# Performance work log

Measured on AMD Instinct MI355X. Metric: run time of the kernel, lower is better.

Reference implementation:

```python
import jax, jax.numpy as jnp
import numpy as np
import math

B, S, KV, D, H = 4, 512, 4096, 1024, 16
HD = D // H  # head_dim = 64


def setup_inputs() -> dict:
    key = jax.random.key(0)
    ks = jax.random.split(key, 12)
    scale = 0.02
    return {
        "x": jax.random.normal(ks[0], (B, S, D), dtype=jnp.float32),
        "xa": jax.random.normal(ks[1], (B, KV, D), dtype=jnp.float32),
        "Wq": jax.random.normal(ks[2], (D, D), dtype=jnp.float32) * scale,
        "bq": jax.random.normal(ks[3], (D,), dtype=jnp.float32) * scale,
        "Wk": jax.random.normal(ks[4], (D, D), dtype=jnp.float32) * scale,  # key has no bias
        "Wv": jax.random.normal(ks[5], (D, D), dtype=jnp.float32) * scale,
        "bv": jax.random.normal(ks[6], (D,), dtype=jnp.float32) * scale,
        "Wo": jax.random.normal(ks[7], (D, D), dtype=jnp.float32) * scale,
        "bo": jax.random.normal(ks[8], (D,), dtype=jnp.float32) * scale,
        "cache_k": jnp.zeros((B, H, KV, HD), dtype=jnp.float32),
        "cache_v": jnp.zeros((B, H, KV, HD), dtype=jnp.float32),
    }


def reference(x, xa, Wq, bq, Wk, Wv, bv, Wo, bo, cache_k, cache_v):
    bsz, seq_len, _ = x.shape
    kv_len = xa.shape[1]
    # projections (torch nn.Linear convention: y = x @ W^T + b)
    q = (x @ Wq.T + bq).reshape(bsz, seq_len, H, HD).transpose(0, 2, 1, 3)   # [B,H,S,HD]
    k = (xa @ Wk.T).reshape(bsz, kv_len, H, HD).transpose(0, 2, 1, 3)        # [B,H,KV,HD]
    v = (xa @ Wv.T + bv).reshape(bsz, kv_len, H, HD).transpose(0, 2, 1, 3)   # [B,H,KV,HD]
    # prefill path: scatter k/v into positions [0, kv_len) of the cache
    updated_k = cache_k.at[:, :, :kv_len, :].set(k)
    updated_v = cache_v.at[:, :, :kv_len, :].set(v)
    # attention over full cache, fp32 softmax as in the original
    scores = jnp.einsum('bhqd,bhkd->bhqk', q, updated_k) / math.sqrt(HD)
    probs = jax.nn.softmax(scores.astype(jnp.float32), axis=-1).astype(q.dtype)
    attn = jnp.einsum('bhqk,bhkd->bhqd', probs, updated_v)                   # [B,H,S,HD]
    attn = attn.transpose(0, 2, 1, 3).reshape(bsz, seq_len, H * HD)
    out = attn @ Wo.T + bo
    return out, updated_k, updated_v
```

## Files before the change

kernel.cpp:

```cpp
#include <hip/hip_runtime.h>
#include <hip/hip_bf16.h>

using u16 = unsigned short;
typedef __bf16 bf16x8 __attribute__((ext_vector_type(8)));
typedef float f32x4 __attribute__((ext_vector_type(4)));

#define SB 4
#define SS 512
#define SKV 4096
#define SD 1024
#define SH 16
#define SHD 64
#define NSPLIT 4
#define NROWS 32768

__device__ inline u16 f2bf(float f){
  __hip_bfloat16 h = __float2bfloat16(f);
  return __builtin_bit_cast(u16, h);
}

__device__ inline bf16x8 ld_frag_g(const u16* p){
  uint4 v = *reinterpret_cast<const uint4*>(p);
  return __builtin_bit_cast(bf16x8, v);
}

__device__ inline bf16x8 ld_frag_lds(const char* base, int ob){
  uint4 v = *reinterpret_cast<const uint4*>(base + ob);
  return __builtin_bit_cast(bf16x8, v);
}

__global__ __launch_bounds__(256) void cast_kernel(const float* __restrict__ src,
                                                   u16* __restrict__ dst, int n4){
  int i = blockIdx.x * 256 + threadIdx.x;
  if (i < n4){
    float4 f = reinterpret_cast<const float4*>(src)[i];
    ushort4 u;
    u.x = f2bf(f.x); u.y = f2bf(f.y); u.z = f2bf(f.z); u.w = f2bf(f.w);
    reinterpret_cast<ushort4*>(dst)[i] = u;
  }
}

enum { MODE_Q = 0, MODE_K = 1, MODE_V = 2, MODE_OUT = 3 };

template<int MODE>
__global__ __launch_bounds__(256) void gemm_bt(const u16* __restrict__ A,
                                               const u16* __restrict__ W,
                                               const float* __restrict__ bias,
                                               float* __restrict__ outF,
                                               u16* __restrict__ outB)
{
  __shared__ u16 As[128*64];
  __shared__ u16 Bs[128*64];
  const int tid  = threadIdx.x;
  const int lane = tid & 63;
  const int wm   = ((tid >> 6) >> 1) * 64;
  const int wn   = ((tid >> 6) & 1) * 64;
  const long rowBase = (long)blockIdx.x * 128;
  const long colBase = (long)blockIdx.y * 128;

  f32x4 acc[4][4];
#pragma unroll
  for (int i = 0; i < 4; i++)
#pragma unroll
    for (int j = 0; j < 4; j++)
      acc[i][j] = (f32x4){0.f, 0.f, 0.f, 0.f};

  for (int kt = 0; kt < 16; ++kt){
    __syncthreads();
#pragma unroll
    for (int i = 0; i < 4; i++){
      int u = tid + i * 256;
      int r = u >> 3, c = u & 7;
      uint4 va = *reinterpret_cast<const uint4*>(A + (rowBase + r) * 1024 + kt * 64 + c * 8);
      uint4 vw = *reinterpret_cast<const uint4*>(W + (colBase + r) * 1024 + kt * 64 + c * 8);
      int ob = (r * 128 + c * 16) ^ ((r & 7) << 4);
      *reinterpret_cast<uint4*>(reinterpret_cast<char*>(As) + ob) = va;
      *reinterpret_cast<uint4*>(reinterpret_cast<char*>(Bs) + ob) = vw;
    }
    __syncthreads();
#pragma unroll
    for (int kk = 0; kk < 2; kk++){
      bf16x8 af[4], bfr[4];
#pragma unroll
      for (int mi = 0; mi < 4; mi++){
        int row = wm + mi * 16 + (lane & 15);
        int ob = (row * 128 + kk * 64 + (lane >> 4) * 16) ^ ((row & 7) << 4);
        af[mi] = __builtin_bit_cast(bf16x8,
                 *reinterpret_cast<const uint4*>(reinterpret_cast<const char*>(As) + ob));
      }
#pragma unroll
      for (int ni = 0; ni < 4; ni++){
        int row = wn + ni * 16 + (lane & 15);
        int ob = (row * 128 + kk * 64 + (lane >> 4) * 16) ^ ((row & 7) << 4);
        bfr[ni] = __builtin_bit_cast(bf16x8,
                 *reinterpret_cast<const uint4*>(reinterpret_cast<const char*>(Bs) + ob));
      }
#pragma unroll
      for (int mi = 0; mi < 4; mi++)
#pragma unroll
        for (int ni = 0; ni < 4; ni++)
          acc[mi][ni] = __builtin_amdgcn_mfma_f32_16x16x32_bf16(af[mi], bfr[ni], acc[mi][ni], 0, 0, 0);
    }
  }

#pragma unroll
  for (int mi = 0; mi < 4; mi++){
#pragma unroll
    for (int ni = 0; ni < 4; ni++){
      long gn = colBase + wn + ni * 16 + (lane & 15);
      float bb = 0.f;
      if (MODE == MODE_Q || MODE == MODE_V || MODE == MODE_OUT) bb = bias[gn];
      if (MODE == MODE_V){
        long gmBase = rowBase + wm + mi * 16 + ((lane >> 4) << 2);
        long b = gmBase >> 12, kv = gmBase & 4095;
        long h = gn >> 6, hd = gn & 63;
        long fidx = ((b * SH + h) * SKV + kv) * SHD + hd;
        ushort4 pk;
        float v0 = acc[mi][ni][0] + bb; outF[fidx          ] = v0; pk.x = f2bf(v0);
        float v1 = acc[mi][ni][1] + bb; outF[fidx +     SHD] = v1; pk.y = f2bf(v1);
        float v2 = acc[mi][ni][2] + bb; outF[fidx + 2 * SHD] = v2; pk.z = f2bf(v2);
        float v3 = acc[mi][ni][3] + bb; outF[fidx + 3 * SHD] = v3; pk.w = f2bf(v3);
        *reinterpret_cast<ushort4*>(outB + ((b * SH + h) * SHD + hd) * SKV + kv) = pk;
      } else {
#pragma unroll
        for (int r = 0; r < 4; r++){
          long gm = rowBase + wm + mi * 16 + ((lane >> 4) << 2) + r;
          float val = acc[mi][ni][r] + bb;
          if (MODE == MODE_OUT){
            outF[gm * 1024 + gn] = val;
          } else if (MODE == MODE_Q){
            long b = gm >> 9, s = gm & 511;
            long h = gn >> 6, hd = gn & 63;
            outB[((b * SH + h) * SS + s) * SHD + hd] = f2bf(val);
          } else {
            long b = gm >> 12, kv = gm & 4095;
            long h = gn >> 6, hd = gn & 63;
            long idx = ((b * SH + h) * SKV + kv) * SHD + hd;
            outF[idx] = val;
            outB[idx] = f2bf(val);
          }
        }
      }
    }
  }
}

__global__ __launch_bounds__(256) void attn_partial(const u16* __restrict__ qb,
                                                    const u16* __restrict__ kb,
                                                    const u16* __restrict__ vTb,
                                                    float* __restrict__ opart,
                                                    float* __restrict__ ml){
  __shared__ u16 Klds[64 * 64];
  __shared__ u16 Vlds[64 * 64];
  __shared__ u16 PT[4][16 * 72];
  const int tid  = threadIdx.x;
  const int lane = tid & 63;
  const int wid  = tid >> 6;
  const int c    = lane & 15;
  const int hi   = lane >> 4;
  const long bh  = blockIdx.x;
  const int  qt  = blockIdx.y;
  const int  split = blockIdx.z;

  const u16* qp = qb + (bh * SS + qt * 64 + wid * 16 + c) * SHD + hi * 8;
  const bf16x8 bq0 = ld_frag_g(qp);
  const bf16x8 bq1 = ld_frag_g(qp + 32);

  f32x4 acc[4];
#pragma unroll
  for (int i = 0; i < 4; i++) acc[i] = (f32x4){0.f, 0.f, 0.f, 0.f};
  float mrun = -INFINITY, lrun = 0.f;

  const u16* kbase = kb  + bh * SKV * SHD;
  const u16* vbase = vTb + bh * SHD * SKV;
  u16* pt = &PT[wid][0];
  char* kch = reinterpret_cast<char*>(Klds);
  char* vch = reinterpret_cast<char*>(Vlds);

  for (int kt = split * 16; kt < split * 16 + 16; ++kt){
    __syncthreads();
#pragma unroll
    for (int i = 0; i < 2; i++){
      int u = tid + i * 256;
      int r = u >> 3, cc = u & 7;
      uint4 kv4 = *reinterpret_cast<const uint4*>(kbase + (kt * 64 + r) * SHD + cc * 8);
      uint4 vv4 = *reinterpret_cast<const uint4*>(vbase + (long)r * SKV + kt * 64 + cc * 8);
      int ob = (r * 128 + cc * 16) ^ ((r & 7) << 4);
      *reinterpret_cast<uint4*>(kch + ob) = kv4;
      *reinterpret_cast<uint4*>(vch + ob) = vv4;
    }
    __syncthreads();

    f32x4 sT[4];
#pragma unroll
    for (int ni = 0; ni < 4; ni++){
      int krow = ni * 16 + c;
      int swz = (krow & 7) << 4;
      int a0 = (krow * 128 + hi * 16) ^ swz;
      int a1 = (krow * 128 + 64 + hi * 16) ^ swz;
      f32x4 z = (f32x4){0.f, 0.f, 0.f, 0.f};
      sT[ni] = __builtin_amdgcn_mfma_f32_16x16x32_bf16(ld_frag_lds(kch, a0), bq0, z, 0, 0, 0);
      sT[ni] = __builtin_amdgcn_mfma_f32_16x16x32_bf16(ld_frag_lds(kch, a1), bq1, sT[ni], 0, 0, 0);
      sT[ni] *= 0.125f;
    }
    f32x4 mv = __builtin_elementwise_max(__builtin_elementwise_max(sT[0], sT[1]),
                                         __builtin_elementwise_max(sT[2], sT[3]));
    float t = fmaxf(fmaxf(mv[0], mv[1]), fmaxf(mv[2], mv[3]));
    t = fmaxf(t, __shfl_xor(t, 16));
    t = fmaxf(t, __shfl_xor(t, 32));
    float mn = fmaxf(mrun, t);
    float al = __expf(mrun - mn);
    f32x4 psv = (f32x4){0.f, 0.f, 0.f, 0.f};
#pragma unroll
    for (int ni = 0; ni < 4; ni++){
      f32x4 p;
      p[0] = __expf(sT[ni][0] - mn); p[1] = __expf(sT[ni][1] - mn);
      p[2] = __expf(sT[ni][2] - mn); p[3] = __expf(sT[ni][3] - mn);
      psv += p;
      ushort4 pk;
      pk.x = f2bf(p[0]); pk.y = f2bf(p[1]); pk.z = f2bf(p[2]); pk.w = f2bf(p[3]);
      *reinterpret_cast<ushort4*>(pt + c * 72 + ni * 16 + hi * 4) = pk;
    }
    float ps = (psv[0] + psv[1]) + (psv[2] + psv[3]);
    ps += __shfl_xor(ps, 16);
    ps += __shfl_xor(ps, 32);
    lrun = lrun * al + ps;
    mrun = mn;
#pragma unroll
    for (int ni = 0; ni < 4; ni++) acc[ni] *= al;
#pragma unroll
    for (int m = 0; m < 2; m++){
      bf16x8 pfrag = __builtin_bit_cast(bf16x8,
          *reinterpret_cast<const uint4*>(pt + c * 72 + m * 32 + hi * 8));
#pragma unroll
      for (int ni = 0; ni < 4; ni++){
        int vrow = ni * 16 + c;
        int av = (vrow * 128 + m * 64 + hi * 16) ^ ((vrow & 7) << 4);
        acc[ni] = __builtin_amdgcn_mfma_f32_16x16x32_bf16(ld_frag_lds(vch, av), pfrag, acc[ni], 0, 0, 0);
      }
    }
  }

  const long row = bh * SS + (long)qt * 64 + wid * 16 + c;
  float* ob = opart + ((long)split * NROWS + row) * SHD;
#pragma unroll
  for (int ni = 0; ni < 4; ni++)
    *reinterpret_cast<f32x4*>(ob + ni * 16 + hi * 4) = acc[ni];
  if (hi == 0){
    ml[(long)split * NROWS + row] = mrun;
    ml[(long)NSPLIT * NROWS + (long)split * NROWS + row] = lrun;
  }
}

__global__ __launch_bounds__(256) void attn_combine(const float* __restrict__ opart,
                                                    const float* __restrict__ ml,
                                                    u16* __restrict__ attnb){
  long idx4 = (long)blockIdx.x * 256 + threadIdx.x;
  long row = idx4 >> 4;
  int  c   = (int)(idx4 & 15);
  float m0 = ml[row], m1 = ml[NROWS + row], m2 = ml[2L*NROWS + row], m3 = ml[3L*NROWS + row];
  float M = fmaxf(fmaxf(m0, m1), fmaxf(m2, m3));
  float w0 = __expf(m0 - M), w1 = __expf(m1 - M), w2 = __expf(m2 - M), w3 = __expf(m3 - M);
  const float* lb = ml + (long)NSPLIT * NROWS;
  float L = w0*lb[row] + w1*lb[NROWS+row] + w2*lb[2L*NROWS+row] + w3*lb[3L*NROWS+row];
  float inv = 1.f / L;
  const float4* op = reinterpret_cast<const float4*>(opart);
  float4 v0 = op[(0L*NROWS + row) * 16 + c];
  float4 v1 = op[(1L*NROWS + row) * 16 + c];
  float4 v2 = op[(2L*NROWS + row) * 16 + c];
  float4 v3 = op[(3L*NROWS + row) * 16 + c];
  float4 val;
  val.x = (w0*v0.x + w1*v1.x + w2*v2.x + w3*v3.x) * inv;
  val.y = (w0*v0.y + w1*v1.y + w2*v2.y + w3*v3.y) * inv;
  val.z = (w0*v0.z + w1*v1.z + w2*v2.z + w3*v3.z) * inv;
  val.w = (w0*v0.w + w1*v1.w + w2*v2.w + w3*v3.w) * inv;
  long bh = row >> 9, s = row & 511;
  long b = bh >> 4, h = bh & 15;
  ushort4 u;
  u.x = f2bf(val.x); u.y = f2bf(val.y); u.z = f2bf(val.z); u.w = f2bf(val.w);
  reinterpret_cast<ushort4*>(attnb)[((b * SS + s) * SD + h * SHD) / 4 + c] = u;
}

extern "C" void kernel_launch(void* const* d_in, const int* in_sizes, int n_in,
                              void* d_out, int out_size, void* d_ws, size_t ws_size,
                              hipStream_t stream)
{
  const float* x  = (const float*)d_in[0];
  const float* xa = (const float*)d_in[1];
  const float* Wq = (const float*)d_in[2];
  const float* bq = (const float*)d_in[3];
  const float* Wk = (const float*)d_in[4];
  const float* Wv = (const float*)d_in[5];
  const float* bv = (const float*)d_in[6];
  const float* Wo = (const float*)d_in[7];
  const float* bo = (const float*)d_in[8];

  float* outO = (float*)d_out;
  float* outK = outO + (long)SB * SS * SD;
  float* outV = outK + (long)SB * SH * SKV * SHD;

  u16* ws   = (u16*)d_ws;
  u16* xb   = ws;
  u16* xab  = xb   + 2097152L;
  u16* Wqb  = xab  + 16777216L;
  u16* Wkb  = Wqb  + 1048576L;
  u16* Wvb  = Wkb  + 1048576L;
  u16* Wob  = Wvb  + 1048576L;
  u16* qbuf = Wob  + 1048576L;
  u16* kbuf = qbuf + 2097152L;
  u16* vTbuf= kbuf + 16777216L;
  u16* mlb  = vTbuf+ 16777216L;

  u16*   attnb = xb;
  float* opart = (float*)xab;
  float* ml    = (float*)mlb;

  auto cast_launch = [&](const float* s, u16* d, long n){
    int n4 = (int)(n / 4);
    cast_kernel<<<(n4 + 255) / 256, 256, 0, stream>>>(s, d, n4);
  };
  cast_launch(x,  xb,  2097152L);
  cast_launch(xa, xab, 16777216L);
  cast_launch(Wq, Wqb, 1048576L);
  cast_launch(Wk, Wkb, 1048576L);
  cast_launch(Wv, Wvb, 1048576L);
  cast_launch(Wo, Wob, 1048576L);

  gemm_bt<MODE_Q>  <<<dim3(16, 8),  256, 0, stream>>>(xb,  Wqb, bq, nullptr, qbuf);
  gemm_bt<MODE_K>  <<<dim3(128, 8), 256, 0, stream>>>(xab, Wkb, nullptr, outK, kbuf);
  gemm_bt<MODE_V>  <<<dim3(128, 8), 256, 0, stream>>>(xab, Wvb, bv, outV, vTbuf);
  attn_partial     <<<dim3(64, 8, NSPLIT), 256, 0, stream>>>(qbuf, kbuf, vTbuf, opart, ml);
  attn_combine     <<<2048, 256, 0, stream>>>(opart, ml, attnb);
  gemm_bt<MODE_OUT><<<dim3(16, 8),  256, 0, stream>>>(attnb, Wob, bo, outO, nullptr);
}
```

Baseline: 275.0 us.

## Store partial attention in bf16, fold softmax scale into Q, swizzle GEMM blocks

Several unrelated changes. Partial attention outputs are now stored and read as bf16 instead of fp32, which halves combine traffic at some cost in precision. The 1/sqrt(d)*log2(e) factor is folded into Q at projection time so softmax can use exp2f with no per-score multiply. The K/V projection GEMMs remap their 1D grid so each XCD works on contiguous row tiles for better L2 reuse, and the four weight casts are merged into one launch.

```diff
diff --git a/kernel.cpp b/kernel.cpp
--- a/kernel.cpp
+++ b/kernel.cpp
@@ -13,10 +13,14 @@
 #define SHD 64
 #define NSPLIT 4
 #define NROWS 32768
+#define QSCALE 0.18033688011112042f
 
 __device__ inline u16 f2bf(float f){
   __hip_bfloat16 h = __float2bfloat16(f);
   return __builtin_bit_cast(u16, h);
+}
+__device__ inline float bf2f(u16 u){
+  return __builtin_bit_cast(float, (unsigned)u << 16);
 }
 
 __device__ inline bf16x8 ld_frag_g(const u16* p){
@@ -40,9 +44,23 @@
   }
 }
 
+__global__ __launch_bounds__(256) void cast_w4(const float* __restrict__ s0,
+                                               const float* __restrict__ s1,
+                                               const float* __restrict__ s2,
+                                               const float* __restrict__ s3,
+                                               u16* __restrict__ dst){
+  int which = blockIdx.x >> 10;
+  int j = (blockIdx.x & 1023) * 256 + threadIdx.x;
+  const float* s = which == 0 ? s0 : which == 1 ? s1 : which == 2 ? s2 : s3;
+  float4 f = reinterpret_cast<const float4*>(s)[j];
+  ushort4 u;
+  u.x = f2bf(f.x); u.y = f2bf(f.y); u.z = f2bf(f.z); u.w = f2bf(f.w);
+  reinterpret_cast<ushort4*>(dst + (long)which * 1048576L)[j] = u;
+}
+
 enum { MODE_Q = 0, MODE_K = 1, MODE_V = 2, MODE_OUT = 3 };
 
-template<int MODE>
+template<int MODE, int SWZ>
 __global__ __launch_bounds__(256) void gemm_bt(const u16* __restrict__ A,
                                                const u16* __restrict__ W,
                                                const float* __restrict__ bias,
@@ -55,8 +73,18 @@
   const int lane = tid & 63;
   const int wm   = ((tid >> 6) >> 1) * 64;
   const int wn   = ((tid >> 6) & 1) * 64;
-  const long rowBase = (long)blockIdx.x * 128;
-  const long colBase = (long)blockIdx.y * 128;
+  long rowBase, colBase;
+  if (SWZ){
+    int lin = blockIdx.x;
+    int xcd = lin & 7, j = lin >> 3;
+    int row = xcd * 16 + (j >> 3);
+    int col = j & 7;
+    rowBase = (long)row * 128;
+    colBase = (long)col * 128;
+  } else {
+    rowBase = (long)blockIdx.x * 128;
+    colBase = (long)blockIdx.y * 128;
+  }
 
   f32x4 acc[4][4];
 #pragma unroll
@@ -85,15 +113,13 @@
       for (int mi = 0; mi < 4; mi++){
         int row = wm + mi * 16 + (lane & 15);
         int ob = (row * 128 + kk * 64 + (lane >> 4) * 16) ^ ((row & 7) << 4);
-        af[mi] = __builtin_bit_cast(bf16x8,
-                 *reinterpret_cast<const uint4*>(reinterpret_cast<const char*>(As) + ob));
+        af[mi] = ld_frag_lds(reinterpret_cast<const char*>(As), ob);
       }
 #pragma unroll
       for (int ni = 0; ni < 4; ni++){
         int row = wn + ni * 16 + (lane & 15);
         int ob = (row * 128 + kk * 64 + (lane >> 4) * 16) ^ ((row & 7) << 4);
-        bfr[ni] = __builtin_bit_cast(bf16x8,
-                 *reinterpret_cast<const uint4*>(reinterpret_cast<const char*>(Bs) + ob));
+        bfr[ni] = ld_frag_lds(reinterpret_cast<const char*>(Bs), ob);
       }
 #pragma unroll
       for (int mi = 0; mi < 4; mi++)
@@ -131,7 +157,7 @@
           } else if (MODE == MODE_Q){
             long b = gm >> 9, s = gm & 511;
             long h = gn >> 6, hd = gn & 63;
-            outB[((b * SH + h) * SS + s) * SHD + hd] = f2bf(val);
+            outB[((b * SH + h) * SS + s) * SHD + hd] = f2bf(val * QSCALE);
           } else {
             long b = gm >> 12, kv = gm & 4095;
             long h = gn >> 6, hd = gn & 63;
@@ -148,7 +174,7 @@
 __global__ __launch_bounds__(256) void attn_partial(const u16* __restrict__ qb,
                                                     const u16* __restrict__ kb,
                                                     const u16* __restrict__ vTb,
-                                                    float* __restrict__ opart,
+                                                    u16* __restrict__ opartB,
                                                     float* __restrict__ ml){
   __shared__ u16 Klds[64 * 64];
   __shared__ u16 Vlds[64 * 64];
@@ -201,7 +227,6 @@
       f32x4 z = (f32x4){0.f, 0.f, 0.f, 0.f};
       sT[ni] = __builtin_amdgcn_mfma_f32_16x16x32_bf16(ld_frag_lds(kch, a0), bq0, z, 0, 0, 0);
       sT[ni] = __builtin_amdgcn_mfma_f32_16x16x32_bf16(ld_frag_lds(kch, a1), bq1, sT[ni], 0, 0, 0);
-      sT[ni] *= 0.125f;
     }
     f32x4 mv = __builtin_elementwise_max(__builtin_elementwise_max(sT[0], sT[1]),
                                          __builtin_elementwise_max(sT[2], sT[3]));
@@ -209,13 +234,13 @@
     t = fmaxf(t, __shfl_xor(t, 16));
     t = fmaxf(t, __shfl_xor(t, 32));
     float mn = fmaxf(mrun, t);
-    float al = __expf(mrun - mn);
+    float al = exp2f(mrun - mn);
     f32x4 psv = (f32x4){0.f, 0.f, 0.f, 0.f};
 #pragma unroll
     for (int ni = 0; ni < 4; ni++){
       f32x4 p;
-      p[0] = __expf(sT[ni][0] - mn); p[1] = __expf(sT[ni][1] - mn);
-      p[2] = __expf(sT[ni][2] - mn); p[3] = __expf(sT[ni][3] - mn);
+      p[0] = exp2f(sT[ni][0] - mn); p[1] = exp2f(sT[ni][1] - mn);
+      p[2] = exp2f(sT[ni][2] - mn); p[3] = exp2f(sT[ni][3] - mn);
       psv += p;
       ushort4 pk;
       pk.x = f2bf(p[0]); pk.y = f2bf(p[1]); pk.z = f2bf(p[2]); pk.w = f2bf(p[3]);
@@ -242,17 +267,21 @@
   }
 
   const long row = bh * SS + (long)qt * 64 + wid * 16 + c;
-  float* ob = opart + ((long)split * NROWS + row) * SHD;
-#pragma unroll
-  for (int ni = 0; ni < 4; ni++)
-    *reinterpret_cast<f32x4*>(ob + ni * 16 + hi * 4) = acc[ni];
+  u16* ob = opartB + ((long)split * NROWS + row) * SHD;
+#pragma unroll
+  for (int ni = 0; ni < 4; ni++){
+    ushort4 pk;
+    pk.x = f2bf(acc[ni][0]); pk.y = f2bf(acc[ni][1]);
+    pk.z = f2bf(acc[ni][2]); pk.w = f2bf(acc[ni][3]);
+    *reinterpret_cast<ushort4*>(ob + ni * 16 + hi * 4) = pk;
+  }
   if (hi == 0){
     ml[(long)split * NROWS + row] = mrun;
     ml[(long)NSPLIT * NROWS + (long)split * NROWS + row] = lrun;
   }
 }
 
-__global__ __launch_bounds__(256) void attn_combine(const float* __restrict__ opart,
+__global__ __launch_bounds__(256) void attn_combine(const u16* __restrict__ opartB,
                                                     const float* __restrict__ ml,
                                                     u16* __restrict__ attnb){
   long idx4 = (long)blockIdx.x * 256 + threadIdx.x;
@@ -260,20 +289,20 @@
   int  c   = (int)(idx4 & 15);
   float m0 = ml[row], m1 = ml[NROWS + row], m2 = ml[2L*NROWS + row], m3 = ml[3L*NROWS + row];
   float M = fmaxf(fmaxf(m0, m1), fmaxf(m2, m3));
-  float w0 = __expf(m0 - M), w1 = __expf(m1 - M), w2 = __expf(m2 - M), w3 = __expf(m3 - M);
+  float w0 = exp2f(m0 - M), w1 = exp2f(m1 - M), w2 = exp2f(m2 - M), w3 = exp2f(m3 - M);
   const float* lb = ml + (long)NSPLIT * NROWS;
   float L = w0*lb[row] + w1*lb[NROWS+row] + w2*lb[2L*NROWS+row] + w3*lb[3L*NROWS+row];
   float inv = 1.f / L;
-  const float4* op = reinterpret_cast<const float4*>(opart);
-  float4 v0 = op[(0L*NROWS + row) * 16 + c];
-  float4 v1 = op[(1L*NROWS + row) * 16 + c];
-  float4 v2 = op[(2L*NROWS + row) * 16 + c];
-  float4 v3 = op[(3L*NROWS + row) * 16 + c];
+  const ushort4* op = reinterpret_cast<const ushort4*>(opartB);
+  ushort4 v0 = op[(0L*NROWS + row) * 16 + c];
+  ushort4 v1 = op[(1L*NROWS + row) * 16 + c];
+  ushort4 v2 = op[(2L*NROWS + row) * 16 + c];
+  ushort4 v3 = op[(3L*NROWS + row) * 16 + c];
   float4 val;
-  val.x = (w0*v0.x + w1*v1.x + w2*v2.x + w3*v3.x) * inv;
-  val.y = (w0*v0.y + w1*v1.y + w2*v2.y + w3*v3.y) * inv;
-  val.z = (w0*v0.z + w1*v1.z + w2*v2.z + w3*v3.z) * inv;
-  val.w = (w0*v0.w + w1*v1.w + w2*v2.w + w3*v3.w) * inv;
+  val.x = (w0*bf2f(v0.x) + w1*bf2f(v1.x) + w2*bf2f(v2.x) + w3*bf2f(v3.x)) * inv;
+  val.y = (w0*bf2f(v0.y) + w1*bf2f(v1.y) + w2*bf2f(v2.y) + w3*bf2f(v3.y)) * inv;
+  val.z = (w0*bf2f(v0.z) + w1*bf2f(v1.z) + w2*bf2f(v2.z) + w3*bf2f(v3.z)) * inv;
+  val.w = (w0*bf2f(v0.w) + w1*bf2f(v1.w) + w2*bf2f(v2.w) + w3*bf2f(v3.w)) * inv;
   long bh = row >> 9, s = row & 511;
   long b = bh >> 4, h = bh & 15;
   ushort4 u;
@@ -311,25 +340,18 @@
   u16* vTbuf= kbuf + 16777216L;
   u16* mlb  = vTbuf+ 16777216L;
 
-  u16*   attnb = xb;
-  float* opart = (float*)xab;
-  float* ml    = (float*)mlb;
-
-  auto cast_launch = [&](const float* s, u16* d, long n){
-    int n4 = (int)(n / 4);
-    cast_kernel<<<(n4 + 255) / 256, 256, 0, stream>>>(s, d, n4);
-  };
-  cast_launch(x,  xb,  2097152L);
-  cast_launch(xa, xab, 16777216L);
-  cast_launch(Wq, Wqb, 1048576L);
-  cast_launch(Wk, Wkb, 1048576L);
-  cast_launch(Wv, Wvb, 1048576L);
-  cast_launch(Wo, Wob, 1048576L);
-
-  gemm_bt<MODE_Q>  <<<dim3(16, 8),  256, 0, stream>>>(xb,  Wqb, bq, nullptr, qbuf);
-  gemm_bt<MODE_K>  <<<dim3(128, 8), 256, 0, stream>>>(xab, Wkb, nullptr, outK, kbuf);
-  gemm_bt<MODE_V>  <<<dim3(128, 8), 256, 0, stream>>>(xab, Wvb, bv, outV, vTbuf);
-  attn_partial     <<<dim3(64, 8, NSPLIT), 256, 0, stream>>>(qbuf, kbuf, vTbuf, opart, ml);
-  attn_combine     <<<2048, 256, 0, stream>>>(opart, ml, attnb);
-  gemm_bt<MODE_OUT><<<dim3(16, 8),  256, 0, stream>>>(attnb, Wob, bo, outO, nullptr);
-}
+  u16*   attnb  = xb;
+  u16*   opartB = xab;
+  float* ml     = (float*)mlb;
+
+  cast_kernel<<<2048, 256, 0, stream>>>(x,  xb,  524288);
+  cast_kernel<<<16384, 256, 0, stream>>>(xa, xab, 4194304);
+  cast_w4    <<<4096, 256, 0, stream>>>(Wq, Wk, Wv, Wo, Wqb);
+
+  gemm_bt<MODE_Q, 0>  <<<dim3(16, 8), 256, 0, stream>>>(xb,  Wqb, bq, nullptr, qbuf);
+  gemm_bt<MODE_K, 1>  <<<1024,        256, 0, stream>>>(xab, Wkb, nullptr, outK, kbuf);
+  gemm_bt<MODE_V, 1>  <<<1024,        256, 0, stream>>>(xab, Wvb, bv, outV, vTbuf);
+  attn_partial        <<<dim3(64, 8, NSPLIT), 256, 0, stream>>>(qbuf, kbuf, vTbuf, opartB, ml);
+  attn_combine        <<<2048, 256, 0, stream>>>(opartB, ml, attnb);
+  gemm_bt<MODE_OUT, 0><<<dim3(16, 8), 256, 0, stream>>>(attnb, Wob, bo, outO, nullptr);
+}
```

Measured after the change: 268.0 us. 2.6% less time.
